# Optimization experiments

Measured on AMD Instinct MI355X. Metric: run time of the kernel, lower is better.

Reference implementation:

```python
import jax, jax.numpy as jnp
import numpy as np

LIDAR_MAX_X = 32.0
LIDAR_MAX_Y = 32.0


def bilinear_grid_sample(value, grid):
    """torch.nn.functional.grid_sample, mode='bilinear', padding_mode='zeros',
    align_corners=False.
    value: (B, C, H, W); grid: (B, Q, P, 2) in [-1, 1] (x=width, y=height).
    Returns (B, C, Q, P)."""
    B, C, H, W = value.shape
    x = (grid[..., 0] + 1.0) * (W / 2) - 0.5  # (B,Q,P) unnormalized col
    y = (grid[..., 1] + 1.0) * (H / 2) - 0.5  # (B,Q,P) unnormalized row
    x0 = jnp.floor(x)
    y0 = jnp.floor(y)
    x1 = x0 + 1.0
    y1 = y0 + 1.0
    wx1 = x - x0
    wx0 = 1.0 - wx1
    wy1 = y - y0
    wy0 = 1.0 - wy1
    vflat = value.reshape(B, C, H * W)

    def gather(ix, iy):
        valid = (ix >= 0) & (ix <= W - 1) & (iy >= 0) & (iy <= H - 1)
        ixc = jnp.clip(ix, 0, W - 1).astype(jnp.int32)
        iyc = jnp.clip(iy, 0, H - 1).astype(jnp.int32)
        idx = iyc * W + ixc  # (B,Q,P)
        g = jax.vmap(lambda v, i: v[:, i])(vflat, idx)  # (B,C,Q,P)
        return g * valid[:, None, :, :].astype(value.dtype)

    out = (gather(x0, y0) * (wx0 * wy0)[:, None]
           + gather(x1, y0) * (wx1 * wy0)[:, None]
           + gather(x0, y1) * (wx0 * wy1)[:, None]
           + gather(x1, y1) * (wx1 * wy1)[:, None])
    return out


def setup_inputs() -> dict:
    key = jax.random.key(0)
    ks = jax.random.split(key, 10)
    bs, Q, P, D = 16, 1024, 8, 256
    Cin, H, W = 64, 128, 128
    queries = jax.random.normal(ks[0], (bs, Q, D), dtype=jnp.float32)
    # scale so trajectory points span the +/-32m BEV extent
    traj_points = jax.random.normal(ks[1], (bs, Q, P, 2), dtype=jnp.float32) * 20.0
    bev_feature = jax.random.normal(ks[2], (bs, Cin, H, W), dtype=jnp.float32)
    spatial_shape = jnp.array([H, W], dtype=jnp.int64)
    attn_w = jax.random.normal(ks[3], (P, D), dtype=jnp.float32) * 0.02
    attn_b = jnp.zeros((P,), dtype=jnp.float32)
    conv_w = jax.random.normal(ks[4], (256, Cin, 3, 3), dtype=jnp.float32) * 0.05
    conv_b = jnp.zeros((256,), dtype=jnp.float32)
    out_w = jax.random.normal(ks[5], (D, D), dtype=jnp.float32) * (1.0 / np.sqrt(D))
    out_b = jnp.zeros((D,), dtype=jnp.float32)
    return {"queries": queries, "traj_points": traj_points,
            "bev_feature": bev_feature, "spatial_shape": spatial_shape,
            "attn_w": attn_w, "attn_b": attn_b,
            "conv_w": conv_w, "conv_b": conv_b,
            "out_w": out_w, "out_b": out_b}


def reference(queries, traj_points, bev_feature, spatial_shape,
              attn_w, attn_b, conv_w, conv_b, out_w, out_b):
    # normalize trajectory to [-1,1] and swap (y,x) -> (x,y) grid order
    grid = jnp.stack([traj_points[..., 1] / LIDAR_MAX_X,
                      traj_points[..., 0] / LIDAR_MAX_Y], axis=-1)  # (bs,Q,P,2)
    # per-query attention over the P sampled points
    attn = jax.nn.softmax(
        jnp.einsum('bqd,pd->bqp', queries, attn_w) + attn_b, axis=-1)  # (bs,Q,P)
    # value projection: 3x3 conv + ReLU
    value = jax.lax.conv_general_dilated(
        bev_feature, conv_w, window_strides=(1, 1),
        padding=((1, 1), (1, 1)),
        dimension_numbers=('NCHW', 'OIHW', 'NCHW'))
    value = jax.nn.relu(value + conv_b[None, :, None, None])  # (bs,256,H,W)
    sampled = bilinear_grid_sample(value, grid)  # (bs,256,Q,P)
    out = jnp.einsum('bcqp,bqp->bqc', sampled, attn)  # weighted sum + permute
    out = jnp.einsum('bqc,dc->bqd', out, out_w) + out_b
    # dropout is identity in eval mode
    return out + queries
```

## Files before the change

kernel.cpp:

```cpp
#include <hip/hip_runtime.h>
#include <stdint.h>


typedef __attribute__((ext_vector_type(8))) short short8;
typedef __attribute__((ext_vector_type(4))) float f32x4;

__device__ __forceinline__ unsigned short f2bf(float f) {
  union { float f; unsigned int u; } v; v.f = f;
  unsigned int r = (v.u + 0x7FFFu + ((v.u >> 16) & 1u)) >> 16;
  return (unsigned short)r;
}
__device__ __forceinline__ float bf2f(unsigned short h) {
  union { unsigned int u; float f; } v; v.u = ((unsigned int)h) << 16;
  return v.f;
}

__device__ __forceinline__ void gload_lds16(const void* g, void* l) {
  __builtin_amdgcn_global_load_lds(
      (const __attribute__((address_space(1))) unsigned int*)g,
      (__attribute__((address_space(3))) unsigned int*)l, 16, 0, 0);
}

__global__ __launch_bounds__(256) void k1_transpose(const float* __restrict__ bev,
                                                    unsigned short* __restrict__ nhwc) {
  __shared__ __align__(16) float lds[64 * 32 * 4];
  const int b = blockIdx.x >> 7, y = blockIdx.x & 127;
  const int t = threadIdx.x;
  const float* src = bev + (size_t)(b * 64) * 16384 + y * 128;
#pragma unroll
  for (int k = 0; k < 8; ++k) {
    int chunk = k * 256 + t;
    int ic = chunk >> 5, xq = chunk & 31;
    float4 v = *(const float4*)(src + ic * 16384 + xq * 4);
    int slot = xq ^ (ic >> 3);
    *(float4*)&lds[(ic * 32 + slot) * 4] = v;
  }
  __syncthreads();
  unsigned short* dst = nhwc + (size_t)blockIdx.x * 8192;
#pragma unroll
  for (int k = 0; k < 4; ++k) {
    int co = k * 256 + t;
    int x = co >> 3, icg = co & 7;
    int slot = (x >> 2) ^ icg;
    int w = x & 3;
    uint4 u;
    unsigned int* up = (unsigned int*)&u;
#pragma unroll
    for (int jj = 0; jj < 4; ++jj) {
      float v0 = lds[((icg * 8 + 2 * jj) * 32 + slot) * 4 + w];
      float v1 = lds[((icg * 8 + 2 * jj + 1) * 32 + slot) * 4 + w];
      up[jj] = (unsigned int)f2bf(v0) | ((unsigned int)f2bf(v1) << 16);
    }
    *(uint4*)(dst + x * 64 + icg * 8) = u;
  }
}

__global__ __launch_bounds__(256) void k1b_pack(const float* __restrict__ conv_w,
                                                const float* __restrict__ out_w,
                                                unsigned short* __restrict__ wconv,
                                                unsigned short* __restrict__ wout,
                                                float* __restrict__ zp) {
  const int tid = blockIdx.x * 256 + threadIdx.x;
  for (int idx = tid; idx < 9 * 8 * 256 * 8; idx += 16384) {
    int j = idx & 7, oc = (idx >> 3) & 255, g = (idx >> 11) & 7, o = idx >> 14;
    wconv[idx] = f2bf(conv_w[(oc * 64 + g * 8 + j) * 9 + o]);
  }
  for (int idx = tid; idx < 32 * 256 * 8; idx += 16384) {
    int j = idx & 7, d = (idx >> 3) & 255, g = idx >> 11;
    wout[idx] = f2bf(out_w[d * 256 + g * 8 + j]);
  }
  if (tid < 64) zp[tid] = 0.0f;
}

#define K2_WOFF 66560
__global__ __launch_bounds__(512, 2) void k2_conv(const unsigned short* __restrict__ nhwc,
                                                  const unsigned short* __restrict__ wconv,
                                                  const float* __restrict__ conv_b,
                                                  const float* __restrict__ zp,
                                                  unsigned short* __restrict__ value) {
  __shared__ __align__(16) char smem[132096];
  const short8* lin = (const short8*)smem;
  const int bid = blockIdx.x;
  const int swz = (bid & 7) * 128 + (bid >> 3);
  const int b = swz >> 6, yp = swz & 63;
  const int y0 = yp * 2;
  const int t = threadIdx.x, wid = t >> 6, lane = t & 63;
  const int wo = wid >> 2, wp = wid & 3;
  const int g = lane >> 4, l15 = lane & 15;
  const int r_hat = wp >> 1;
  const int xbase = (wp & 1) * 64 + l15;

  const unsigned short* bevb = nhwc + (size_t)b * (128 * 128 * 64);
  for (int i = wid; i < 65; i += 8) {
    const int chunk = i * 64 + lane;
    const int ridx = chunk / 1040;
    const int rem = chunk - ridx * 1040;
    const int icg = rem / 130;
    const int c = rem - icg * 130;
    const int yy = y0 - 1 + ridx, xx = c - 1;
    const void* src = (yy >= 0 && yy < 128 && xx >= 0 && xx < 128)
                          ? (const void*)(bevb + ((yy * 128 + xx) * 64 + icg * 8))
                          : (const void*)zp;
    gload_lds16(src, smem + i * 1024);
  }
#pragma unroll
  for (int s0 = 0; s0 < 3; ++s0) {
    const unsigned short* wsrc = wconv + (size_t)s0 * 1024 * 8;
    char* wdst = smem + K2_WOFF + s0 * 16384 + wid * 2048;
    gload_lds16(wsrc + (size_t)(wid * 128 + lane) * 8, wdst);
    gload_lds16(wsrc + (size_t)(wid * 128 + 64 + lane) * 8, wdst + 1024);
  }
  asm volatile("s_waitcnt vmcnt(4)" ::: "memory");
  __builtin_amdgcn_s_barrier();

  const f32x4 z4 = {0.f, 0.f, 0.f, 0.f};
  f32x4 acc[8][4];
#pragma unroll
  for (int i = 0; i < 8; ++i)
#pragma unroll
    for (int j = 0; j < 4; ++j) acc[i][j] = z4;

#pragma unroll
  for (int s = 0; s < 18; ++s) {
    const int o = s >> 1, ich = s & 1;
    const int dyr = o / 3;
    const int dx = o - dyr * 3 - 1;
    if (s + 3 <= 17) {
      const int s1 = s + 3;
      const unsigned short* wsrc = wconv + (size_t)s1 * 1024 * 8;
      char* wdst = smem + K2_WOFF + (s1 & 3) * 16384 + wid * 2048;
      gload_lds16(wsrc + (size_t)(wid * 128 + lane) * 8, wdst);
      gload_lds16(wsrc + (size_t)(wid * 128 + 64 + lane) * 8, wdst + 1024);
    }
    const short8* wb = (const short8*)(smem + K2_WOFF + (s & 3) * 16384);
    short8 af[8];
#pragma unroll
    for (int ocf = 0; ocf < 8; ++ocf) af[ocf] = wb[g * 256 + wo * 128 + ocf * 16 + l15];
    short8 bf[4];
    const int cb = ((r_hat + dyr) * 8 + ich * 4 + g) * 130 + xbase + 1 + dx;
#pragma unroll
    for (int pf = 0; pf < 4; ++pf) bf[pf] = lin[cb + pf * 16];
    __builtin_amdgcn_s_setprio(1);
#pragma unroll
    for (int ocf = 0; ocf < 8; ++ocf)
#pragma unroll
      for (int pf = 0; pf < 4; ++pf)
        acc[ocf][pf] = __builtin_amdgcn_mfma_f32_16x16x32_bf16(af[ocf], bf[pf], acc[ocf][pf], 0, 0, 0);
    __builtin_amdgcn_s_setprio(0);
    if (s < 15)       asm volatile("s_waitcnt vmcnt(4)" ::: "memory");
    else if (s == 15) asm volatile("s_waitcnt vmcnt(2)" ::: "memory");
    else if (s == 16) asm volatile("s_waitcnt vmcnt(0)" ::: "memory");
    if (s < 17) __builtin_amdgcn_s_barrier();
  }

  const int y = y0 + r_hat;
  unsigned short* vrow = value + (((size_t)(b * 128 + y) * 128 + xbase) * 256);
#pragma unroll
  for (int ocf = 0; ocf < 8; ++ocf) {
    const int ocb = wo * 128 + ocf * 16 + g * 4;
    const float4 cb4 = *(const float4*)(conv_b + ocb);
#pragma unroll
    for (int pf = 0; pf < 4; ++pf) {
      ushort4 ov;
      float v0 = acc[ocf][pf][0] + cb4.x; ov.x = f2bf(v0 > 0.f ? v0 : 0.f);
      float v1 = acc[ocf][pf][1] + cb4.y; ov.y = f2bf(v1 > 0.f ? v1 : 0.f);
      float v2 = acc[ocf][pf][2] + cb4.z; ov.z = f2bf(v2 > 0.f ? v2 : 0.f);
      float v3 = acc[ocf][pf][3] + cb4.w; ov.w = f2bf(v3 > 0.f ? v3 : 0.f);
      *(ushort4*)(vrow + (size_t)pf * 16 * 256 + ocb) = ov;
    }
  }
}

__global__ __launch_bounds__(256) void k3_sample(const float* __restrict__ queries,
                                                 const float* __restrict__ traj,
                                                 const float* __restrict__ attn_w,
                                                 const float* __restrict__ attn_b,
                                                 const unsigned short* __restrict__ value,
                                                 unsigned short* __restrict__ S) {
  const int wid = threadIdx.x >> 6, lane = threadIdx.x & 63;
  const int qg = blockIdx.x * 4 + wid;
  const int b = qg >> 10;
  const float4 qv = ((const float4*)queries)[qg * 64 + lane];
  float a[8];
#pragma unroll
  for (int p = 0; p < 8; ++p) {
    float4 wv = ((const float4*)attn_w)[p * 64 + lane];
    float d = qv.x * wv.x + qv.y * wv.y + qv.z * wv.z + qv.w * wv.w;
#pragma unroll
    for (int off = 32; off >= 1; off >>= 1) d += __shfl_xor(d, off);
    a[p] = d + attn_b[p];
  }
  float mx = a[0];
#pragma unroll
  for (int p = 1; p < 8; ++p) mx = fmaxf(mx, a[p]);
  float ssum = 0.f;
#pragma unroll
  for (int p = 0; p < 8; ++p) { a[p] = __expf(a[p] - mx); ssum += a[p]; }
  const float inv = 1.f / ssum;

  float acc0 = 0.f, acc1 = 0.f, acc2 = 0.f, acc3 = 0.f;
  const unsigned short* vb = value + (size_t)b * (128 * 128 * 256);
  const int coff = lane * 4;
#pragma unroll
  for (int p = 0; p < 8; ++p) {
    const float ty = traj[(qg * 8 + p) * 2 + 0];
    const float tx = traj[(qg * 8 + p) * 2 + 1];
    const float fx = (tx * 0.03125f + 1.f) * 64.f - 0.5f;
    const float fy = (ty * 0.03125f + 1.f) * 64.f - 0.5f;
    const float fx0 = floorf(fx), fy0 = floorf(fy);
    const int ix0 = (int)fx0, iy0 = (int)fy0;
    const float wx1 = fx - fx0, wx0 = 1.f - wx1;
    const float wy1 = fy - fy0, wy0 = 1.f - wy1;
    const float ap = a[p] * inv;
    const float cw[4] = {wx0 * wy0 * ap, wx1 * wy0 * ap, wx0 * wy1 * ap, wx1 * wy1 * ap};
    const int cx[4] = {ix0, ix0 + 1, ix0, ix0 + 1};
    const int cy[4] = {iy0, iy0, iy0 + 1, iy0 + 1};
#pragma unroll
    for (int cc = 0; cc < 4; ++cc) {
      if (cx[cc] >= 0 && cx[cc] < 128 && cy[cc] >= 0 && cy[cc] < 128) {
        const ushort4 v = *(const ushort4*)(vb + (cy[cc] * 128 + cx[cc]) * 256 + coff);
        acc0 += cw[cc] * bf2f(v.x);
        acc1 += cw[cc] * bf2f(v.y);
        acc2 += cw[cc] * bf2f(v.z);
        acc3 += cw[cc] * bf2f(v.w);
      }
    }
  }
  ushort4 o;
  o.x = f2bf(acc0); o.y = f2bf(acc1); o.z = f2bf(acc2); o.w = f2bf(acc3);
  *(ushort4*)(S + (size_t)qg * 256 + coff) = o;
}

__global__ __launch_bounds__(256, 2) void k4_proj(const unsigned short* __restrict__ S,
                                                  const unsigned short* __restrict__ wout,
                                                  const float* __restrict__ out_b,
                                                  const float* __restrict__ queries,
                                                  float* __restrict__ out) {
  __shared__ __align__(16) char smem[16384];
  const short8* lds8 = (const short8*)smem;
  const short8* wp8 = (const short8*)wout;
  const int t = threadIdx.x, wid = t >> 6, lane = t & 63;
  const int wo = wid >> 1, wq = wid & 1;
  const int q0 = blockIdx.x * 128;
  const int g = lane >> 4, l15 = lane & 15;
  const f32x4 z4 = {0.f, 0.f, 0.f, 0.f};
  f32x4 acc[8][4];
#pragma unroll
  for (int i = 0; i < 8; ++i)
#pragma unroll
    for (int j = 0; j < 4; ++j) acc[i][j] = z4;

#pragma unroll
  for (int ii = 0; ii < 2; ++ii) {
    const int chunk = wid * 128 + ii * 64 + lane;
    const int gg = chunk >> 7, q = chunk & 127;
    gload_lds16(S + ((size_t)(q0 + q) * 256 + gg * 8), smem + wid * 2048 + ii * 1024);
  }
  __syncthreads();

#pragma unroll
  for (int ks = 0; ks < 8; ++ks) {
    if (ks < 7) {
      const int k1 = ks + 1;
#pragma unroll
      for (int ii = 0; ii < 2; ++ii) {
        const int chunk = wid * 128 + ii * 64 + lane;
        const int gg = chunk >> 7, q = chunk & 127;
        gload_lds16(S + ((size_t)(q0 + q) * 256 + k1 * 32 + gg * 8),
                    smem + ((k1 & 1) ? 8192 : 0) + wid * 2048 + ii * 1024);
      }
    }
    short8 af[8];
#pragma unroll
    for (int df = 0; df < 8; ++df)
      af[df] = wp8[(ks * 4 + g) * 256 + wo * 128 + df * 16 + l15];
    short8 bf[4];
    const short8* sb = lds8 + ((ks & 1) ? 512 : 0);
#pragma unroll
    for (int qf = 0; qf < 4; ++qf) bf[qf] = sb[g * 128 + wq * 64 + qf * 16 + l15];
    __builtin_amdgcn_s_setprio(1);
#pragma unroll
    for (int df = 0; df < 8; ++df)
#pragma unroll
      for (int qf = 0; qf < 4; ++qf)
        acc[df][qf] = __builtin_amdgcn_mfma_f32_16x16x32_bf16(af[df], bf[qf], acc[df][qf], 0, 0, 0);
    __builtin_amdgcn_s_setprio(0);
    __syncthreads();
  }

#pragma unroll
  for (int df = 0; df < 8; ++df) {
    const int db = wo * 128 + df * 16 + g * 4;
    const float4 ob4 = *(const float4*)(out_b + db);
#pragma unroll
    for (int qf = 0; qf < 4; ++qf) {
      const int q = q0 + wq * 64 + qf * 16 + l15;
      const float4 qv = *(const float4*)(queries + (size_t)q * 256 + db);
      float4 ov;
      ov.x = acc[df][qf][0] + ob4.x + qv.x;
      ov.y = acc[df][qf][1] + ob4.y + qv.y;
      ov.z = acc[df][qf][2] + ob4.z + qv.z;
      ov.w = acc[df][qf][3] + ob4.w + qv.w;
      *(float4*)(out + (size_t)q * 256 + db) = ov;
    }
  }
}

extern "C" void kernel_launch(void* const* d_in, const int* in_sizes, int n_in,
                              void* d_out, int out_size, void* d_ws, size_t ws_size,
                              hipStream_t stream) {
  const float* queries = (const float*)d_in[0];
  const float* traj    = (const float*)d_in[1];
  const float* bev     = (const float*)d_in[2];
  const float* attn_w  = (const float*)d_in[4];
  const float* attn_b  = (const float*)d_in[5];
  const float* conv_w  = (const float*)d_in[6];
  const float* conv_b  = (const float*)d_in[7];
  const float* out_w   = (const float*)d_in[8];
  const float* out_b   = (const float*)d_in[9];
  float* out = (float*)d_out;

  char* ws = (char*)d_ws;
  unsigned short* bev_nhwc = (unsigned short*)(ws);
  unsigned short* value    = (unsigned short*)(ws + 33554432);
  unsigned short* wconv    = (unsigned short*)(ws + 167772160);
  unsigned short* wout     = (unsigned short*)(ws + 168067072);
  unsigned short* Sbuf     = (unsigned short*)(ws + 168198144);
  float*          zp       = (float*)(ws + 176586752);

  k1_transpose<<<2048, 256, 0, stream>>>(bev, bev_nhwc);
  k1b_pack<<<64, 256, 0, stream>>>(conv_w, out_w, wconv, wout, zp);
  k2_conv<<<1024, 512, 0, stream>>>(bev_nhwc, wconv, conv_b, zp, value);
  k3_sample<<<4096, 256, 0, stream>>>(queries, traj, attn_w, attn_b, value, Sbuf);
  k4_proj<<<128, 256, 0, stream>>>(Sbuf, wout, out_b, queries, out);
}
```

Baseline: 175.3 us.

## Enlarge per-wave conv tile to 8x8 MFMA fragments with register double-buffering

Changes the conv kernel from 8 waves with 8x4 MFMA tiles to 4 waves with 8x8 tiles, each covering a full 128-pixel row half. This raises operand reuse per LDS read. It also software-pipelines the loop so the next stage's A/B fragments are read from LDS while the current MFMAs run. The cost is far more accumulator and operand registers and only one 256-thread block per CU, which cuts occupancy and latency hiding.

Measured after the change: 184.1 us. 1.05x slower.

```diff
diff --git a/kernel.cpp b/kernel.cpp
--- a/kernel.cpp
+++ b/kernel.cpp
@@ -73,7 +73,39 @@
 }
 
 #define K2_WOFF 66560
-__global__ __launch_bounds__(512, 2) void k2_conv(const unsigned short* __restrict__ nhwc,
+
+#define K2_STAGE(s1) do {                                                     \
+    const unsigned short* wsrc_ = wconv + (size_t)(s1) * 8192;                \
+    char* wdst_ = smem + K2_WOFF + ((s1) & 3) * 16384;                        \
+    _Pragma("unroll")                                                         \
+    for (int j_ = 0; j_ < 4; ++j_)                                            \
+      gload_lds16(wsrc_ + (size_t)((wid * 4 + j_) * 64 + lane) * 8,           \
+                  wdst_ + (wid * 4 + j_) * 1024);                             \
+  } while (0)
+
+#define K2_READ(sr, A, B) do {                                                \
+    const short8* wb_ = (const short8*)(smem + K2_WOFF + ((sr) & 3) * 16384); \
+    _Pragma("unroll")                                                         \
+    for (int ocf_ = 0; ocf_ < 8; ++ocf_) A[ocf_] = wb_[aoff + ocf_ * 16];     \
+    const int o_ = (sr) >> 1, ich_ = (sr) & 1;                                \
+    const int dyr_ = o_ / 3, dx_ = o_ - dyr_ * 3 - 1;                         \
+    const int cb_ = ((rh + dyr_) * 8 + ich_ * 4 + g) * 130 + 1 + dx_ + l15;   \
+    _Pragma("unroll")                                                         \
+    for (int pf_ = 0; pf_ < 8; ++pf_) B[pf_] = lin[cb_ + pf_ * 16];           \
+  } while (0)
+
+#define K2_MFMA(A, B) do {                                                    \
+    __builtin_amdgcn_s_setprio(1);                                            \
+    _Pragma("unroll")                                                         \
+    for (int ocf_ = 0; ocf_ < 8; ++ocf_)                                      \
+      _Pragma("unroll")                                                       \
+      for (int pf_ = 0; pf_ < 8; ++pf_)                                       \
+        acc[ocf_][pf_] = __builtin_amdgcn_mfma_f32_16x16x32_bf16(             \
+            A[ocf_], B[pf_], acc[ocf_][pf_], 0, 0, 0);                        \
+    __builtin_amdgcn_s_setprio(0);                                            \
+  } while (0)
+
+__global__ __launch_bounds__(256, 1) void k2_conv(const unsigned short* __restrict__ nhwc,
                                                   const unsigned short* __restrict__ wconv,
                                                   const float* __restrict__ conv_b,
                                                   const float* __restrict__ zp,
@@ -85,13 +117,12 @@
   const int b = swz >> 6, yp = swz & 63;
   const int y0 = yp * 2;
   const int t = threadIdx.x, wid = t >> 6, lane = t & 63;
-  const int wo = wid >> 2, wp = wid & 3;
+  const int wo = wid >> 1, rh = wid & 1;
   const int g = lane >> 4, l15 = lane & 15;
-  const int r_hat = wp >> 1;
-  const int xbase = (wp & 1) * 64 + l15;
+  const int aoff = g * 256 + wo * 128 + l15;
 
   const unsigned short* bevb = nhwc + (size_t)b * (128 * 128 * 64);
-  for (int i = wid; i < 65; i += 8) {
+  for (int i = wid; i < 65; i += 4) {
     const int chunk = i * 64 + lane;
     const int ridx = chunk / 1040;
     const int rem = chunk - ridx * 1040;
@@ -103,64 +134,56 @@
                           : (const void*)zp;
     gload_lds16(src, smem + i * 1024);
   }
-#pragma unroll
-  for (int s0 = 0; s0 < 3; ++s0) {
-    const unsigned short* wsrc = wconv + (size_t)s0 * 1024 * 8;
-    char* wdst = smem + K2_WOFF + s0 * 16384 + wid * 2048;
-    gload_lds16(wsrc + (size_t)(wid * 128 + lane) * 8, wdst);
-    gload_lds16(wsrc + (size_t)(wid * 128 + 64 + lane) * 8, wdst + 1024);
-  }
+  K2_STAGE(0);
+  K2_STAGE(1);
+  K2_STAGE(2);
   asm volatile("s_waitcnt vmcnt(4)" ::: "memory");
   __builtin_amdgcn_s_barrier();
 
   const f32x4 z4 = {0.f, 0.f, 0.f, 0.f};
-  f32x4 acc[8][4];
+  f32x4 acc[8][8];
 #pragma unroll
   for (int i = 0; i < 8; ++i)
 #pragma unroll
-    for (int j = 0; j < 4; ++j) acc[i][j] = z4;
-
-#pragma unroll
-  for (int s = 0; s < 18; ++s) {
-    const int o = s >> 1, ich = s & 1;
-    const int dyr = o / 3;
-    const int dx = o - dyr * 3 - 1;
-    if (s + 3 <= 17) {
-      const int s1 = s + 3;
-      const unsigned short* wsrc = wconv + (size_t)s1 * 1024 * 8;
-      char* wdst = smem + K2_WOFF + (s1 & 3) * 16384 + wid * 2048;
-      gload_lds16(wsrc + (size_t)(wid * 128 + lane) * 8, wdst);
-      gload_lds16(wsrc + (size_t)(wid * 128 + 64 + lane) * 8, wdst + 1024);
-    }
-    const short8* wb = (const short8*)(smem + K2_WOFF + (s & 3) * 16384);
-    short8 af[8];
-#pragma unroll
-    for (int ocf = 0; ocf < 8; ++ocf) af[ocf] = wb[g * 256 + wo * 128 + ocf * 16 + l15];
-    short8 bf[4];
-    const int cb = ((r_hat + dyr) * 8 + ich * 4 + g) * 130 + xbase + 1 + dx;
-#pragma unroll
-    for (int pf = 0; pf < 4; ++pf) bf[pf] = lin[cb + pf * 16];
-    __builtin_amdgcn_s_setprio(1);
-#pragma unroll
-    for (int ocf = 0; ocf < 8; ++ocf)
-#pragma unroll
-      for (int pf = 0; pf < 4; ++pf)
-        acc[ocf][pf] = __builtin_amdgcn_mfma_f32_16x16x32_bf16(af[ocf], bf[pf], acc[ocf][pf], 0, 0, 0);
-    __builtin_amdgcn_s_setprio(0);
-    if (s < 15)       asm volatile("s_waitcnt vmcnt(4)" ::: "memory");
-    else if (s == 15) asm volatile("s_waitcnt vmcnt(2)" ::: "memory");
-    else if (s == 16) asm volatile("s_waitcnt vmcnt(0)" ::: "memory");
-    if (s < 17) __builtin_amdgcn_s_barrier();
-  }
-
-  const int y = y0 + r_hat;
-  unsigned short* vrow = value + (((size_t)(b * 128 + y) * 128 + xbase) * 256);
+    for (int j = 0; j < 8; ++j) acc[i][j] = z4;
+
+  short8 aC[8], bC[8], aN[8], bN[8];
+  K2_READ(0, aC, bC);
+
+  for (int it = 0; it < 7; ++it) {
+    const int s0 = 2 * it, s1 = 2 * it + 1;
+    K2_STAGE(s0 + 3);
+    K2_READ(s0 + 1, aN, bN);
+    K2_MFMA(aC, bC);
+    asm volatile("s_waitcnt vmcnt(4)" ::: "memory");
+    __builtin_amdgcn_s_barrier();
+    K2_STAGE(s1 + 3);
+    K2_READ(s1 + 1, aC, bC);
+    K2_MFMA(aN, bN);
+    asm volatile("s_waitcnt vmcnt(4)" ::: "memory");
+    __builtin_amdgcn_s_barrier();
+  }
+  K2_STAGE(17);
+  K2_READ(15, aN, bN);
+  K2_MFMA(aC, bC);
+  asm volatile("s_waitcnt vmcnt(4)" ::: "memory");
+  __builtin_amdgcn_s_barrier();
+  K2_READ(16, aC, bC);
+  K2_MFMA(aN, bN);
+  asm volatile("s_waitcnt vmcnt(0)" ::: "memory");
+  __builtin_amdgcn_s_barrier();
+  K2_READ(17, aN, bN);
+  K2_MFMA(aC, bC);
+  K2_MFMA(aN, bN);
+
+  const int y = y0 + rh;
+  unsigned short* vrow = value + (((size_t)(b * 128 + y) * 128 + l15) * 256);
 #pragma unroll
   for (int ocf = 0; ocf < 8; ++ocf) {
     const int ocb = wo * 128 + ocf * 16 + g * 4;
     const float4 cb4 = *(const float4*)(conv_b + ocb);
 #pragma unroll
-    for (int pf = 0; pf < 4; ++pf) {
+    for (int pf = 0; pf < 8; ++pf) {
       ushort4 ov;
       float v0 = acc[ocf][pf][0] + cb4.x; ov.x = f2bf(v0 > 0.f ? v0 : 0.f);
       float v1 = acc[ocf][pf][1] + cb4.y; ov.y = f2bf(v1 > 0.f ? v1 : 0.f);
@@ -330,7 +353,7 @@
 
   k1_transpose<<<2048, 256, 0, stream>>>(bev, bev_nhwc);
   k1b_pack<<<64, 256, 0, stream>>>(conv_w, out_w, wconv, wout, zp);
-  k2_conv<<<1024, 512, 0, stream>>>(bev_nhwc, wconv, conv_b, zp, value);
+  k2_conv<<<1024, 256, 0, stream>>>(bev_nhwc, wconv, conv_b, zp, value);
   k3_sample<<<4096, 256, 0, stream>>>(queries, traj, attn_w, attn_b, value, Sbuf);
   k4_proj<<<128, 256, 0, stream>>>(Sbuf, wout, out_b, queries, out);
 }
```
